# Performance work log

Measured on AMD Instinct MI355X. Metric: run time of the kernel, lower is better.

Reference implementation:

```python
import jax, jax.numpy as jnp
import numpy as np

N = 50000      # nodes
E = 800000     # edges
D_IN = 128     # input feature dim
HID = 64       # out_channels (per-head dim; concat=False -> head mean)
HEADS = 2
NEG_SLOPE = 0.2


def gat_layer(x, src, dst, Ws, Wd, a_s, a_d, b):
    # PyG GATConv, add_self_loops=False, concat=False (mean over heads)
    n = x.shape[0]
    H, C = a_s.shape
    hs = (x @ Ws).reshape(n, H, C)          # source-side features [N,H,C]
    hd = (x @ Wd).reshape(n, H, C)          # dest-side features   [N,H,C]
    als = (hs * a_s).sum(-1)                # [N,H]
    ald = (hd * a_d).sum(-1)                # [N,H]
    e = jax.nn.leaky_relu(als[src] + ald[dst], NEG_SLOPE)   # [E,H]
    # segment softmax over edges grouped by destination node
    m = jax.ops.segment_max(e, dst, num_segments=n)
    m = jax.lax.stop_gradient(jnp.where(jnp.isfinite(m), m, 0.0))
    ex = jnp.exp(e - m[dst])
    den = jax.ops.segment_sum(ex, dst, num_segments=n)
    alpha = ex / (den[dst] + 1e-16)                          # [E,H]
    out = jax.ops.segment_sum(hs[src] * alpha[:, :, None], dst, num_segments=n)
    return out.mean(axis=1) + b             # [N,C]


def setup_inputs() -> dict:
    key = jax.random.key(0)
    ks = jax.random.split(key, 32)
    d = {}
    d["x"] = jax.random.normal(ks[0], (N, D_IN), jnp.float32)
    d["edge_index"] = jax.random.randint(ks[1], (2, E), 0, N, jnp.int32)
    dins = [D_IN, HID, HID]
    i = 2
    for l in range(1, 4):
        din = dins[l - 1]
        s = 1.0 / np.sqrt(din)
        d[f"Ws{l}"] = jax.random.normal(ks[i], (din, HEADS * HID), jnp.float32) * s; i += 1
        d[f"Wd{l}"] = jax.random.normal(ks[i], (din, HEADS * HID), jnp.float32) * s; i += 1
        d[f"as{l}"] = jax.random.normal(ks[i], (HEADS, HID), jnp.float32) * 0.1; i += 1
        d[f"ad{l}"] = jax.random.normal(ks[i], (HEADS, HID), jnp.float32) * 0.1; i += 1
        d[f"b{l}"] = jnp.zeros((HID,), jnp.float32)
        d[f"Wl{l}"] = jax.random.normal(ks[i], (din, HID), jnp.float32) * s; i += 1
        d[f"bl{l}"] = jnp.zeros((HID,), jnp.float32)
    return d


def reference(x, edge_index,
              Ws1, Wd1, as1, ad1, b1, Wl1, bl1,
              Ws2, Wd2, as2, ad2, b2, Wl2, bl2,
              Ws3, Wd3, as3, ad3, b3, Wl3, bl3):
    src, dst = edge_index[0], edge_index[1]
    h = jax.nn.relu(gat_layer(x, src, dst, Ws1, Wd1, as1, ad1, b1) + x @ Wl1 + bl1)
    h = jax.nn.relu(gat_layer(h, src, dst, Ws2, Wd2, as2, ad2, b2) + h @ Wl2 + bl2)
    h = jax.nn.relu(gat_layer(h, src, dst, Ws3, Wd3, as3, ad3, b3) + h @ Wl3 + bl3)
    return h
```

## Files before the change

### kernel.cpp

```cpp
#include <hip/hip_runtime.h>
#include <hip/hip_bf16.h>

#define NN 50000
#define NE 800000
#define SCAN_BS 1024
#define SCAN_NB ((NN + SCAN_BS - 1) / SCAN_BS)
#define EB ((NE + 255) / 256)
#define GB ((NN + 63) / 64)
#define RB ((NN + 1 + 255) / 256)

typedef __attribute__((ext_vector_type(8))) __bf16 bf16x8;
typedef __attribute__((ext_vector_type(4))) float float4v;

__device__ __forceinline__ unsigned pack_bf2(float lo, float hi) {
    union { __bf16 b; unsigned short u; } a, c;
    a.b = (__bf16)lo; c.b = (__bf16)hi;
    return (unsigned)a.u | ((unsigned)c.u << 16);
}
__device__ __forceinline__ float2 unpack_bf2(unsigned v) {
    union { unsigned short u; __bf16 b; } lo, hi;
    lo.u = (unsigned short)(v & 0xffff); hi.u = (unsigned short)(v >> 16);
    return make_float2((float)lo.b, (float)hi.b);
}


__device__ __forceinline__ void convert_w_part(const float* __restrict__ Ws,
                                               const float* __restrict__ Wd,
                                               const float* __restrict__ Wl,
                                               __bf16* __restrict__ Wt, int NC, int i)
{
    if (i >= NC * 23040) return;
    int chunk = i / 23040, rem = i % 23040;
    int r = rem / 72, c = rem % 72;
    float v = 0.f;
    if (c < 64) {
        int k = chunk * 64 + c;
        if (r < 128)      v = Ws[k * 128 + r];
        else if (r < 256) v = Wd[k * 128 + (r - 128)];
        else              v = Wl[k * 64 + (r - 256)];
    }
    Wt[i] = (__bf16)v;
}

__global__ void __launch_bounds__(256)
prep_kernel(const int* __restrict__ ei, int* __restrict__ deg, int* __restrict__ rank,
            const float* __restrict__ Ws1, const float* __restrict__ Wd1,
            const float* __restrict__ Wl1, __bf16* __restrict__ Wt1,
            const float* __restrict__ Ws2, const float* __restrict__ Wd2,
            const float* __restrict__ Wl2, __bf16* __restrict__ Wt2,
            const float* __restrict__ Ws3, const float* __restrict__ Wd3,
            const float* __restrict__ Wl3, __bf16* __restrict__ Wt3)
{
    int bi = blockIdx.x;
    if (bi < EB) {
        int e = bi * 256 + threadIdx.x;
        if (e < NE) rank[e] = atomicAdd(&deg[ei[NE + e]], 1);
    } else if (bi < EB + 180) {
        convert_w_part(Ws1, Wd1, Wl1, Wt1, 2, (bi - EB) * 256 + threadIdx.x);
    } else if (bi < EB + 270) {
        convert_w_part(Ws2, Wd2, Wl2, Wt2, 1, (bi - EB - 180) * 256 + threadIdx.x);
    } else {
        convert_w_part(Ws3, Wd3, Wl3, Wt3, 1, (bi - EB - 270) * 256 + threadIdx.x);
    }
}


__global__ void __launch_bounds__(SCAN_BS)
scan12_kernel(const int* __restrict__ deg, int* __restrict__ exl,
              int* __restrict__ bsum, int* __restrict__ boff, int* __restrict__ ticket)
{
    __shared__ int sh[SCAN_BS];
    __shared__ int lastFlag;
    int t = threadIdx.x;
    int i = blockIdx.x * SCAN_BS + t;
    int v = (i < NN) ? deg[i] : 0;
    sh[t] = v;
    __syncthreads();
    for (int off = 1; off < SCAN_BS; off <<= 1) {
        int u = (t >= off) ? sh[t - off] : 0;
        __syncthreads();
        sh[t] += u;
        __syncthreads();
    }
    if (i < NN) exl[i] = sh[t] - v;
    if (t == SCAN_BS - 1) {
        bsum[blockIdx.x] = sh[t];
        __threadfence();
        lastFlag = (atomicAdd(ticket, 1) == SCAN_NB - 1);
    }
    __syncthreads();
    if (lastFlag && t < 64) {
        __threadfence();
        int l = t;
        int bv = (l < SCAN_NB) ? bsum[l] : 0;
        int own = bv;
        for (int off = 1; off < 64; off <<= 1) {
            int u = __shfl_up(bv, off);
            if (l >= off) bv += u;
        }
        if (l < SCAN_NB) boff[l] = bv - own;
    }
}


__global__ void __launch_bounds__(256)
csr_finish(const int* __restrict__ ei, const int* __restrict__ rank,
           const int* __restrict__ exl, const int* __restrict__ boff,
           int* __restrict__ row, int* __restrict__ csr_src)
{
    int bi = blockIdx.x;
    if (bi < RB) {
        int i = bi * 256 + threadIdx.x;
        if (i < NN)       row[i] = exl[i] + boff[i >> 10];
        else if (i == NN) row[i] = NE;
    } else {
        int e = (bi - RB) * 256 + threadIdx.x;
        if (e < NE) {
            int s = ei[e], d = ei[NE + e];
            csr_src[exl[d] + boff[d >> 10] + rank[e]] = s;
        }
    }
}


__device__ __forceinline__ bf16x8 load_af(const __bf16* p) { return *(const bf16x8*)p; }
__device__ __forceinline__ bf16x8 load_af(const float* p) {
    float4 u = *(const float4*)p;
    float4 v = *(const float4*)(p + 4);
    bf16x8 r;
    r[0] = (__bf16)u.x; r[1] = (__bf16)u.y; r[2] = (__bf16)u.z; r[3] = (__bf16)u.w;
    r[4] = (__bf16)v.x; r[5] = (__bf16)v.y; r[6] = (__bf16)v.z; r[7] = (__bf16)v.w;
    return r;
}

template <int K, typename TIN>
__global__ void __launch_bounds__(256, 4)
mfma_gemm(const TIN* __restrict__ xin, const __bf16* __restrict__ Wt,
          const float* __restrict__ a_s, const float* __restrict__ a_d,
          unsigned* __restrict__ hsb, float* __restrict__ lin,
          float* __restrict__ als, float* __restrict__ ald)
{
    constexpr int NPH = (K / 64) * 2;
    __shared__ __align__(16) char ldsW[160 * 144];

    const int tid  = threadIdx.x;
    const int lane = tid & 63;
    const int wave = tid >> 6;
    const int l15 = lane & 15, quad = lane >> 4;
    const int n0 = blockIdx.x * 64 + wave * 16;
    const int nA = min(n0 + l15, NN - 1);

    bf16x8 afr[K / 32];
#pragma unroll
    for (int ks = 0; ks < K / 32; ++ks)
        afr[ks] = load_af(xin + (size_t)nA * K + ks * 32 + quad * 8);

    const uint4* gW = (const uint4*)Wt;
    uint4* lw = (uint4*)ldsW;
    uint4 st[6];

#pragma unroll
    for (int i = 0; i < 6; ++i) { int idx = i * 256 + tid; if (idx < 1440) st[i] = gW[idx]; }

    float4v acc[20];
#pragma unroll
    for (int t = 0; t < 20; ++t) acc[t] = (float4v){0.f, 0.f, 0.f, 0.f};

#pragma unroll
    for (int ph = 0; ph < NPH; ++ph) {
        if (ph) __syncthreads();
#pragma unroll
        for (int i = 0; i < 6; ++i) { int idx = i * 256 + tid; if (idx < 1440) lw[idx] = st[i]; }
        __syncthreads();
        if (ph + 1 < NPH) {
            const uint4* gs = gW + (ph + 1) * 1440;
#pragma unroll
            for (int i = 0; i < 6; ++i) { int idx = i * 256 + tid; if (idx < 1440) st[i] = gs[idx]; }
        }
        const int hh = ph & 1, ch = ph >> 1;
#pragma unroll
        for (int ksh = 0; ksh < 2; ++ksh) {
#pragma unroll
            for (int tl = 0; tl < 10; ++tl) {
                bf16x8 bw = *(const bf16x8*)&ldsW[(tl * 16 + l15) * 144 + (ksh * 4 + quad) * 16];
                acc[hh * 10 + tl] =
                    __builtin_amdgcn_mfma_f32_16x16x32_bf16(bw, afr[ch * 2 + ksh], acc[hh * 10 + tl], 0, 0, 0);
            }
        }
    }

    float s0 = 0.f, s1 = 0.f, d0 = 0.f, d1 = 0.f;
#pragma unroll
    for (int t = 0; t < 4; ++t) {
        float4 as0 = *(const float4*)&a_s[t * 16 + quad * 4];
        float4 as1 = *(const float4*)&a_s[64 + t * 16 + quad * 4];
        float4 ad0 = *(const float4*)&a_d[t * 16 + quad * 4];
        float4 ad1 = *(const float4*)&a_d[64 + t * 16 + quad * 4];
        s0 += acc[t][0] * as0.x + acc[t][1] * as0.y + acc[t][2] * as0.z + acc[t][3] * as0.w;
        s1 += acc[t + 4][0] * as1.x + acc[t + 4][1] * as1.y + acc[t + 4][2] * as1.z + acc[t + 4][3] * as1.w;
        d0 += acc[t + 8][0] * ad0.x + acc[t + 8][1] * ad0.y + acc[t + 8][2] * ad0.z + acc[t + 8][3] * ad0.w;
        d1 += acc[t + 12][0] * ad1.x + acc[t + 12][1] * ad1.y + acc[t + 12][2] * ad1.z + acc[t + 12][3] * ad1.w;
    }
    s0 += __shfl_xor(s0, 16); s0 += __shfl_xor(s0, 32);
    s1 += __shfl_xor(s1, 16); s1 += __shfl_xor(s1, 32);
    d0 += __shfl_xor(d0, 16); d0 += __shfl_xor(d0, 32);
    d1 += __shfl_xor(d1, 16); d1 += __shfl_xor(d1, 32);

    int n = n0 + l15;
    if (n < NN) {
#pragma unroll
        for (int t = 0; t < 4; ++t) {
            uint4 u;
            u.x = pack_bf2(acc[t][0], acc[t + 4][0]);
            u.y = pack_bf2(acc[t][1], acc[t + 4][1]);
            u.z = pack_bf2(acc[t][2], acc[t + 4][2]);
            u.w = pack_bf2(acc[t][3], acc[t + 4][3]);
            *(uint4*)&hsb[(size_t)n * 64 + t * 16 + quad * 4] = u;
            *(float4*)&lin[(size_t)n * 64 + t * 16 + quad * 4] =
                make_float4(acc[16 + t][0], acc[16 + t][1], acc[16 + t][2], acc[16 + t][3]);
        }
        if (quad == 0) *(float2*)&als[(size_t)n * 2] = make_float2(s0, s1);
        if (quad == 1) *(float2*)&ald[(size_t)n * 2] = make_float2(d0, d1);
    }
}


__device__ __forceinline__ float2 edge_w(const float* __restrict__ als, int s,
                                         float ad0, float ad1)
{
    float2 al = *(const float2*)&als[s * 2];
    float e0 = al.x + ad0; e0 = (e0 >= 0.f) ? e0 : 0.2f * e0;
    float e1 = al.y + ad1; e1 = (e1 >= 0.f) ? e1 : 0.2f * e1;
    return make_float2(__expf(e0), __expf(e1));
}

__device__ __forceinline__ void store_q(float* p, float v0, float v1, float v2, float v3) {
    *(float4*)p = make_float4(v0, v1, v2, v3);
}
__device__ __forceinline__ void store_q(__bf16* p, float v0, float v1, float v2, float v3) {
    *(uint2*)p = make_uint2(pack_bf2(v0, v1), pack_bf2(v2, v3));
}

template <typename TO>
__global__ void __launch_bounds__(256, 8)
gat_aggregate(const int* __restrict__ row, const int* __restrict__ csr_src,
              const float* __restrict__ als, const float* __restrict__ ald,
              const unsigned* __restrict__ hsb, const float* __restrict__ lin,
              const float* __restrict__ b, const float* __restrict__ bl,
              TO* __restrict__ out)
{
    int w = (blockIdx.x * 256 + threadIdx.x) >> 6;
    int lane = threadIdx.x & 63;
    int q = lane >> 4;
    int l15 = lane & 15;
    if (w >= NN) return;
    int p0 = row[w], p1 = row[w + 1];
    float ad0 = ald[w * 2 + 0];
    float ad1 = ald[w * 2 + 1];

    float a0[4] = {0.f, 0.f, 0.f, 0.f};
    float a1[4] = {0.f, 0.f, 0.f, 0.f};
    float den0 = 0.f, den1 = 0.f;

    for (int p = p0 + q; p < p1; p += 16) {
#pragma unroll
        for (int j = 0; j < 4; ++j) {
            int pp = p + 4 * j;
            bool live = (pp < p1);
            int s = csr_src[live ? pp : p0];
            float2 e = edge_w(als, s, ad0, ad1);
            if (!live) e = make_float2(0.f, 0.f);
            uint4 g = *(const uint4*)&hsb[(size_t)s * 64 + 4 * l15];
            den0 += e.x; den1 += e.y;
            float2 h;
            h = unpack_bf2(g.x); a0[0] += e.x * h.x; a1[0] += e.y * h.y;
            h = unpack_bf2(g.y); a0[1] += e.x * h.x; a1[1] += e.y * h.y;
            h = unpack_bf2(g.z); a0[2] += e.x * h.x; a1[2] += e.y * h.y;
            h = unpack_bf2(g.w); a0[3] += e.x * h.x; a1[3] += e.y * h.y;
        }
    }

#pragma unroll
    for (int i = 0; i < 4; ++i) {
        a0[i] += __shfl_xor(a0[i], 16); a0[i] += __shfl_xor(a0[i], 32);
        a1[i] += __shfl_xor(a1[i], 16); a1[i] += __shfl_xor(a1[i], 32);
    }
    den0 += __shfl_xor(den0, 16); den0 += __shfl_xor(den0, 32);
    den1 += __shfl_xor(den1, 16); den1 += __shfl_xor(den1, 32);

    if (q == 0) {
        int c0 = 4 * l15;
        float r0 = 1.f / (den0 + 1e-16f);
        float r1 = 1.f / (den1 + 1e-16f);
        float4 lv = *(const float4*)&lin[(size_t)w * 64 + c0];
        float v0 = 0.5f * (a0[0] * r0 + a1[0] * r1) + b[c0 + 0] + bl[c0 + 0] + lv.x;
        float v1 = 0.5f * (a0[1] * r0 + a1[1] * r1) + b[c0 + 1] + bl[c0 + 1] + lv.y;
        float v2 = 0.5f * (a0[2] * r0 + a1[2] * r1) + b[c0 + 2] + bl[c0 + 2] + lv.z;
        float v3 = 0.5f * (a0[3] * r0 + a1[3] * r1) + b[c0 + 3] + bl[c0 + 3] + lv.w;
        store_q(&out[(size_t)w * 64 + c0],
                fmaxf(v0, 0.f), fmaxf(v1, 0.f), fmaxf(v2, 0.f), fmaxf(v3, 0.f));
    }
}


extern "C" void kernel_launch(void* const* d_in, const int* in_sizes, int n_in,
                              void* d_out, int out_size, void* d_ws, size_t ws_size,
                              hipStream_t stream)
{
    const float* x  = (const float*)d_in[0];
    const int*   ei = (const int*)d_in[1];
    const float* Ws[3]; const float* Wd[3]; const float* As[3]; const float* Ad[3];
    const float* Bb[3]; const float* Wl[3]; const float* Bl[3];
    for (int l = 0; l < 3; ++l) {
        int base = 2 + 7 * l;
        Ws[l] = (const float*)d_in[base + 0];
        Wd[l] = (const float*)d_in[base + 1];
        As[l] = (const float*)d_in[base + 2];
        Ad[l] = (const float*)d_in[base + 3];
        Bb[l] = (const float*)d_in[base + 4];
        Wl[l] = (const float*)d_in[base + 5];
        Bl[l] = (const float*)d_in[base + 6];
    }

    float* ws = (float*)d_ws;
    unsigned* hsb = (unsigned*)ws;
    float* lin  = (float*)(hsb + (size_t)NN * 64);
    float* als  = lin + (size_t)NN * 64;
    float* ald  = als + (size_t)NN * 2;
    __bf16* hb  = (__bf16*)(ald + (size_t)NN * 2);
    __bf16* Wt1 = hb + (size_t)NN * 64;
    __bf16* Wt2 = Wt1 + 2 * 320 * 72;
    __bf16* Wt3 = Wt2 + 320 * 72;
    int* row     = (int*)(Wt3 + 320 * 72);
    int* deg     = row + (NN + 1);
    int* ticket  = deg + NN;
    int* rank    = ticket + 1;
    int* exl     = rank + NE;
    int* bsum    = exl + NN;
    int* boff    = bsum + SCAN_NB;
    int* csr_src = boff + SCAN_NB;

    const int WB = (NN * 64 + 255) / 256;

    hipMemsetAsync(deg, 0, sizeof(int) * (NN + 1), stream);
    prep_kernel<<<EB + 360, 256, 0, stream>>>(ei, deg, rank,
        Ws[0], Wd[0], Wl[0], Wt1,
        Ws[1], Wd[1], Wl[1], Wt2,
        Ws[2], Wd[2], Wl[2], Wt3);
    scan12_kernel<<<SCAN_NB, SCAN_BS, 0, stream>>>(deg, exl, bsum, boff, ticket);
    csr_finish<<<RB + EB, 256, 0, stream>>>(ei, rank, exl, boff, row, csr_src);

    for (int l = 0; l < 3; ++l) {
        if (l == 0) {
            mfma_gemm<128, float><<<GB, 256, 0, stream>>>(
                x, Wt1, As[0], Ad[0], hsb, lin, als, ald);
        } else {
            const __bf16* wt = (l == 1) ? Wt2 : Wt3;
            mfma_gemm<64, __bf16><<<GB, 256, 0, stream>>>(
                hb, wt, As[l], Ad[l], hsb, lin, als, ald);
        }
        if (l == 2) {
            gat_aggregate<float><<<WB, 256, 0, stream>>>(
                row, csr_src, als, ald, hsb, lin, Bb[l], Bl[l], (float*)d_out);
        } else {
            gat_aggregate<__bf16><<<WB, 256, 0, stream>>>(
                row, csr_src, als, ald, hsb, lin, Bb[l], Bl[l], hb);
        }
    }
}
```

Baseline: 365.5 us.

## Fuse all stages into one persistent cooperative mega-kernel with grid syncs

Replaces the memset plus separate prep, scan, CSR-finish, GEMM and aggregation launches with a single cooperative kernel that walks each stage with grid-stride loops separated by grid.sync. Layer-1 GEMM is co-scheduled with the CSR row/scatter phase, and the block-offset scan becomes a serial single-thread pass. This removes launch gaps and tail idling between kernels, at the cost of grid-wide barrier overhead and occupancy being capped by the GEMM's register/LDS needs for the aggregation phases as well.

Measured after the change: 1.040 ms. 185% more time.

```diff
diff --git a/kernel.cpp b/kernel.cpp
--- a/kernel.cpp
+++ b/kernel.cpp
@@ -1,13 +1,18 @@
 #include <hip/hip_runtime.h>
 #include <hip/hip_bf16.h>
+#include <hip/hip_cooperative_groups.h>
+
+namespace cg = cooperative_groups;
 
 #define NN 50000
 #define NE 800000
-#define SCAN_BS 1024
-#define SCAN_NB ((NN + SCAN_BS - 1) / SCAN_BS)
-#define EB ((NE + 255) / 256)
-#define GB ((NN + 63) / 64)
-#define RB ((NN + 1 + 255) / 256)
+#define NCH 196
+#define CVU 360
+#define ZU  196
+#define EBU 3125
+#define GBU 782
+#define RBU 196
+#define AGU 12500
 
 typedef __attribute__((ext_vector_type(8))) __bf16 bf16x8;
 typedef __attribute__((ext_vector_type(4))) float float4v;
@@ -23,13 +28,21 @@
     return make_float2((float)lo.b, (float)hi.b);
 }
 
+struct MegaArgs {
+    const float* x; const int* ei;
+    const float* Ws[3]; const float* Wd[3]; const float* Wl[3];
+    const float* as[3]; const float* ad[3]; const float* bb[3]; const float* bl[3];
+    __bf16* Wt1; __bf16* Wt2; __bf16* Wt3;
+    unsigned* hsb; float* lin; float* als; float* ald; __bf16* hb;
+    int* row; int* deg; int* rank; int* exl; int* bsum; int* boff; int* csr_src;
+    float* out;
+};
 
 __device__ __forceinline__ void convert_w_part(const float* __restrict__ Ws,
                                                const float* __restrict__ Wd,
                                                const float* __restrict__ Wl,
-                                               __bf16* __restrict__ Wt, int NC, int i)
-{
-    if (i >= NC * 23040) return;
+                                               __bf16* __restrict__ Wt, int i)
+{
     int chunk = i / 23040, rem = i % 23040;
     int r = rem / 72, c = rem % 72;
     float v = 0.f;
@@ -42,87 +55,6 @@
     Wt[i] = (__bf16)v;
 }
 
-__global__ void __launch_bounds__(256)
-prep_kernel(const int* __restrict__ ei, int* __restrict__ deg, int* __restrict__ rank,
-            const float* __restrict__ Ws1, const float* __restrict__ Wd1,
-            const float* __restrict__ Wl1, __bf16* __restrict__ Wt1,
-            const float* __restrict__ Ws2, const float* __restrict__ Wd2,
-            const float* __restrict__ Wl2, __bf16* __restrict__ Wt2,
-            const float* __restrict__ Ws3, const float* __restrict__ Wd3,
-            const float* __restrict__ Wl3, __bf16* __restrict__ Wt3)
-{
-    int bi = blockIdx.x;
-    if (bi < EB) {
-        int e = bi * 256 + threadIdx.x;
-        if (e < NE) rank[e] = atomicAdd(&deg[ei[NE + e]], 1);
-    } else if (bi < EB + 180) {
-        convert_w_part(Ws1, Wd1, Wl1, Wt1, 2, (bi - EB) * 256 + threadIdx.x);
-    } else if (bi < EB + 270) {
-        convert_w_part(Ws2, Wd2, Wl2, Wt2, 1, (bi - EB - 180) * 256 + threadIdx.x);
-    } else {
-        convert_w_part(Ws3, Wd3, Wl3, Wt3, 1, (bi - EB - 270) * 256 + threadIdx.x);
-    }
-}
-
-
-__global__ void __launch_bounds__(SCAN_BS)
-scan12_kernel(const int* __restrict__ deg, int* __restrict__ exl,
-              int* __restrict__ bsum, int* __restrict__ boff, int* __restrict__ ticket)
-{
-    __shared__ int sh[SCAN_BS];
-    __shared__ int lastFlag;
-    int t = threadIdx.x;
-    int i = blockIdx.x * SCAN_BS + t;
-    int v = (i < NN) ? deg[i] : 0;
-    sh[t] = v;
-    __syncthreads();
-    for (int off = 1; off < SCAN_BS; off <<= 1) {
-        int u = (t >= off) ? sh[t - off] : 0;
-        __syncthreads();
-        sh[t] += u;
-        __syncthreads();
-    }
-    if (i < NN) exl[i] = sh[t] - v;
-    if (t == SCAN_BS - 1) {
-        bsum[blockIdx.x] = sh[t];
-        __threadfence();
-        lastFlag = (atomicAdd(ticket, 1) == SCAN_NB - 1);
-    }
-    __syncthreads();
-    if (lastFlag && t < 64) {
-        __threadfence();
-        int l = t;
-        int bv = (l < SCAN_NB) ? bsum[l] : 0;
-        int own = bv;
-        for (int off = 1; off < 64; off <<= 1) {
-            int u = __shfl_up(bv, off);
-            if (l >= off) bv += u;
-        }
-        if (l < SCAN_NB) boff[l] = bv - own;
-    }
-}
-
-
-__global__ void __launch_bounds__(256)
-csr_finish(const int* __restrict__ ei, const int* __restrict__ rank,
-           const int* __restrict__ exl, const int* __restrict__ boff,
-           int* __restrict__ row, int* __restrict__ csr_src)
-{
-    int bi = blockIdx.x;
-    if (bi < RB) {
-        int i = bi * 256 + threadIdx.x;
-        if (i < NN)       row[i] = exl[i] + boff[i >> 10];
-        else if (i == NN) row[i] = NE;
-    } else {
-        int e = (bi - RB) * 256 + threadIdx.x;
-        if (e < NE) {
-            int s = ei[e], d = ei[NE + e];
-            csr_src[exl[d] + boff[d >> 10] + rank[e]] = s;
-        }
-    }
-}
-
-
 __device__ __forceinline__ bf16x8 load_af(const __bf16* p) { return *(const bf16x8*)p; }
 __device__ __forceinline__ bf16x8 load_af(const float* p) {
     float4 u = *(const float4*)p;
@@ -134,20 +66,18 @@
 }
 
 template <int K, typename TIN>
-__global__ void __launch_bounds__(256, 4)
-mfma_gemm(const TIN* __restrict__ xin, const __bf16* __restrict__ Wt,
-          const float* __restrict__ a_s, const float* __restrict__ a_d,
-          unsigned* __restrict__ hsb, float* __restrict__ lin,
-          float* __restrict__ als, float* __restrict__ ald)
+__device__ __forceinline__ void gemm_tile(int item, const TIN* __restrict__ xin,
+        const __bf16* __restrict__ Wt,
+        const float* __restrict__ a_s, const float* __restrict__ a_d,
+        unsigned* __restrict__ hsb, float* __restrict__ lin,
+        float* __restrict__ als, float* __restrict__ ald, char* ldsW)
 {
     constexpr int NPH = (K / 64) * 2;
-    __shared__ __align__(16) char ldsW[160 * 144];
-
     const int tid  = threadIdx.x;
     const int lane = tid & 63;
     const int wave = tid >> 6;
     const int l15 = lane & 15, quad = lane >> 4;
-    const int n0 = blockIdx.x * 64 + wave * 16;
+    const int n0 = item * 64 + wave * 16;
     const int nA = min(n0 + l15, NN - 1);
 
     bf16x8 afr[K / 32];
@@ -168,7 +98,7 @@
 
 #pragma unroll
     for (int ph = 0; ph < NPH; ++ph) {
-        if (ph) __syncthreads();
+        __syncthreads();
 #pragma unroll
         for (int i = 0; i < 6; ++i) { int idx = i * 256 + tid; if (idx < 1440) lw[idx] = st[i]; }
         __syncthreads();
@@ -188,6 +118,7 @@
             }
         }
     }
+    __syncthreads();
 
     float s0 = 0.f, s1 = 0.f, d0 = 0.f, d1 = 0.f;
 #pragma unroll
@@ -224,7 +155,6 @@
     }
 }
 
-
 __device__ __forceinline__ float2 edge_w(const float* __restrict__ als, int s,
                                          float ad0, float ad1)
 {
@@ -233,7 +163,6 @@
     float e1 = al.y + ad1; e1 = (e1 >= 0.f) ? e1 : 0.2f * e1;
     return make_float2(__expf(e0), __expf(e1));
 }
-
 __device__ __forceinline__ void store_q(float* p, float v0, float v1, float v2, float v3) {
     *(float4*)p = make_float4(v0, v1, v2, v3);
 }
@@ -242,18 +171,16 @@
 }
 
 template <typename TO>
-__global__ void __launch_bounds__(256, 8)
-gat_aggregate(const int* __restrict__ row, const int* __restrict__ csr_src,
-              const float* __restrict__ als, const float* __restrict__ ald,
-              const unsigned* __restrict__ hsb, const float* __restrict__ lin,
-              const float* __restrict__ b, const float* __restrict__ bl,
-              TO* __restrict__ out)
-{
-    int w = (blockIdx.x * 256 + threadIdx.x) >> 6;
+__device__ __forceinline__ void agg_node(int w,
+        const int* __restrict__ row, const int* __restrict__ csr_src,
+        const float* __restrict__ als, const float* __restrict__ ald,
+        const unsigned* __restrict__ hsb, const float* __restrict__ lin,
+        const float* __restrict__ b, const float* __restrict__ bl,
+        TO* __restrict__ out)
+{
     int lane = threadIdx.x & 63;
     int q = lane >> 4;
     int l15 = lane & 15;
-    if (w >= NN) return;
     int p0 = row[w], p1 = row[w + 1];
     float ad0 = ald[w * 2 + 0];
     float ad1 = ald[w * 2 + 1];
@@ -302,69 +229,158 @@
     }
 }
 
+__global__ void __launch_bounds__(256, 4)
+mega_kernel(MegaArgs A)
+{
+    __shared__ __align__(16) char lds[160 * 144];
+    cg::grid_group grid = cg::this_grid();
+    const int G = gridDim.x;
+    const int tid = threadIdx.x;
+
+    for (int u = blockIdx.x; u < CVU + ZU; u += G) {
+        if (u < CVU) {
+            int i = u * 256 + tid;
+            if (i < 46080)      convert_w_part(A.Ws[0], A.Wd[0], A.Wl[0], A.Wt1, i);
+            else if (i < 69120) convert_w_part(A.Ws[1], A.Wd[1], A.Wl[1], A.Wt2, i - 46080);
+            else                convert_w_part(A.Ws[2], A.Wd[2], A.Wl[2], A.Wt3, i - 69120);
+        } else {
+            int i = (u - CVU) * 256 + tid;
+            if (i < NN) A.deg[i] = 0;
+        }
+    }
+    grid.sync();
+
+    for (int u = blockIdx.x; u < EBU; u += G) {
+        int e = u * 256 + tid;
+        if (e < NE) A.rank[e] = atomicAdd(&A.deg[A.ei[NE + e]], 1);
+    }
+    grid.sync();
+
+    {
+        int* sh = (int*)lds;
+        for (int u = blockIdx.x; u < NCH; u += G) {
+            int i = u * 256 + tid;
+            int v = (i < NN) ? A.deg[i] : 0;
+            sh[tid] = v;
+            __syncthreads();
+            for (int off = 1; off < 256; off <<= 1) {
+                int t = (tid >= off) ? sh[tid - off] : 0;
+                __syncthreads();
+                sh[tid] += t;
+                __syncthreads();
+            }
+            if (i < NN) A.exl[i] = sh[tid] - v;
+            if (tid == 255) A.bsum[u] = sh[255];
+            __syncthreads();
+        }
+    }
+    grid.sync();
+
+    if (blockIdx.x == 0 && tid == 0) {
+        int run = 0;
+        for (int c = 0; c < NCH; ++c) { A.boff[c] = run; run += A.bsum[c]; }
+    }
+    grid.sync();
+
+    for (int u = blockIdx.x; u < GBU + RBU + EBU; u += G) {
+        if (u < GBU) {
+            gemm_tile<128, float>(u, A.x, A.Wt1, A.as[0], A.ad[0],
+                                  A.hsb, A.lin, A.als, A.ald, lds);
+        } else if (u < GBU + RBU) {
+            int i = (u - GBU) * 256 + tid;
+            if (i < NN)       A.row[i] = A.exl[i] + A.boff[i >> 8];
+            else if (i == NN) A.row[i] = NE;
+        } else {
+            int e = (u - GBU - RBU) * 256 + tid;
+            if (e < NE) {
+                int s = A.ei[e], d = A.ei[NE + e];
+                A.csr_src[A.exl[d] + A.boff[d >> 8] + A.rank[e]] = s;
+            }
+        }
+    }
+    grid.sync();
+
+    for (int u = blockIdx.x; u < AGU; u += G) {
+        int w = u * 4 + (tid >> 6);
+        if (w < NN) agg_node<__bf16>(w, A.row, A.csr_src, A.als, A.ald,
+                                     A.hsb, A.lin, A.bb[0], A.bl[0], A.hb);
+    }
+    grid.sync();
+
+    for (int u = blockIdx.x; u < GBU; u += G)
+        gemm_tile<64, __bf16>(u, A.hb, A.Wt2, A.as[1], A.ad[1],
+                              A.hsb, A.lin, A.als, A.ald, lds);
+    grid.sync();
+
+    for (int u = blockIdx.x; u < AGU; u += G) {
+        int w = u * 4 + (tid >> 6);
+        if (w < NN) agg_node<__bf16>(w, A.row, A.csr_src, A.als, A.ald,
+                                     A.hsb, A.lin, A.bb[1], A.bl[1], A.hb);
+    }
+    grid.sync();
+
+    for (int u = blockIdx.x; u < GBU; u += G)
+        gemm_tile<64, __bf16>(u, A.hb, A.Wt3, A.as[2], A.ad[2],
+                              A.hsb, A.lin, A.als, A.ald, lds);
+    grid.sync();
+
+    for (int u = blockIdx.x; u < AGU; u += G) {
+        int w = u * 4 + (tid >> 6);
+        if (w < NN) agg_node<float>(w, A.row, A.csr_src, A.als, A.ald,
+                                    A.hsb, A.lin, A.bb[2], A.bl[2], A.out);
+    }
+}
+
 
 extern "C" void kernel_launch(void* const* d_in, const int* in_sizes, int n_in,
                               void* d_out, int out_size, void* d_ws, size_t ws_size,
                               hipStream_t stream)
 {
-    const float* x  = (const float*)d_in[0];
-    const int*   ei = (const int*)d_in[1];
-    const float* Ws[3]; const float* Wd[3]; const float* As[3]; const float* Ad[3];
-    const float* Bb[3]; const float* Wl[3]; const float* Bl[3];
+    MegaArgs A;
+    A.x  = (const float*)d_in[0];
+    A.ei = (const int*)d_in[1];
     for (int l = 0; l < 3; ++l) {
         int base = 2 + 7 * l;
-        Ws[l] = (const float*)d_in[base + 0];
-        Wd[l] = (const float*)d_in[base + 1];
-        As[l] = (const float*)d_in[base + 2];
-        Ad[l] = (const float*)d_in[base + 3];
-        Bb[l] = (const float*)d_in[base + 4];
-        Wl[l] = (const float*)d_in[base + 5];
-        Bl[l] = (const float*)d_in[base + 6];
+        A.Ws[l] = (const float*)d_in[base + 0];
+        A.Wd[l] = (const float*)d_in[base + 1];
+        A.as[l] = (const float*)d_in[base + 2];
+        A.ad[l] = (const float*)d_in[base + 3];
+        A.bb[l] = (const float*)d_in[base + 4];
+        A.Wl[l] = (const float*)d_in[base + 5];
+        A.bl[l] = (const float*)d_in[base + 6];
     }
 
     float* ws = (float*)d_ws;
-    unsigned* hsb = (unsigned*)ws;
-    float* lin  = (float*)(hsb + (size_t)NN * 64);
-    float* als  = lin + (size_t)NN * 64;
-    float* ald  = als + (size_t)NN * 2;
-    __bf16* hb  = (__bf16*)(ald + (size_t)NN * 2);
-    __bf16* Wt1 = hb + (size_t)NN * 64;
-    __bf16* Wt2 = Wt1 + 2 * 320 * 72;
-    __bf16* Wt3 = Wt2 + 320 * 72;
-    int* row     = (int*)(Wt3 + 320 * 72);
-    int* deg     = row + (NN + 1);
-    int* ticket  = deg + NN;
-    int* rank    = ticket + 1;
-    int* exl     = rank + NE;
-    int* bsum    = exl + NN;
-    int* boff    = bsum + SCAN_NB;
-    int* csr_src = boff + SCAN_NB;
-
-    const int WB = (NN * 64 + 255) / 256;
-
-    hipMemsetAsync(deg, 0, sizeof(int) * (NN + 1), stream);
-    prep_kernel<<<EB + 360, 256, 0, stream>>>(ei, deg, rank,
-        Ws[0], Wd[0], Wl[0], Wt1,
-        Ws[1], Wd[1], Wl[1], Wt2,
-        Ws[2], Wd[2], Wl[2], Wt3);
-    scan12_kernel<<<SCAN_NB, SCAN_BS, 0, stream>>>(deg, exl, bsum, boff, ticket);
-    csr_finish<<<RB + EB, 256, 0, stream>>>(ei, rank, exl, boff, row, csr_src);
-
-    for (int l = 0; l < 3; ++l) {
-        if (l == 0) {
-            mfma_gemm<128, float><<<GB, 256, 0, stream>>>(
-                x, Wt1, As[0], Ad[0], hsb, lin, als, ald);
-        } else {
-            const __bf16* wt = (l == 1) ? Wt2 : Wt3;
-            mfma_gemm<64, __bf16><<<GB, 256, 0, stream>>>(
-                hb, wt, As[l], Ad[l], hsb, lin, als, ald);
-        }
-        if (l == 2) {
-            gat_aggregate<float><<<WB, 256, 0, stream>>>(
-                row, csr_src, als, ald, hsb, lin, Bb[l], Bl[l], (float*)d_out);
-        } else {
-            gat_aggregate<__bf16><<<WB, 256, 0, stream>>>(
-                row, csr_src, als, ald, hsb, lin, Bb[l], Bl[l], hb);
-        }
-    }
-}
+    A.hsb = (unsigned*)ws;
+    A.lin = (float*)(A.hsb + (size_t)NN * 64);
+    A.als = A.lin + (size_t)NN * 64;
+    A.ald = A.als + (size_t)NN * 2;
+    A.hb  = (__bf16*)(A.ald + (size_t)NN * 2);
+    A.Wt1 = A.hb + (size_t)NN * 64;
+    A.Wt2 = A.Wt1 + 2 * 320 * 72;
+    A.Wt3 = A.Wt2 + 320 * 72;
+    A.row = (int*)(A.Wt3 + 320 * 72);
+    A.deg = A.row + (NN + 1);
+    A.rank = A.deg + NN;
+    A.exl  = A.rank + NE;
+    A.bsum = A.exl + NN;
+    A.boff = A.bsum + NCH;
+    A.csr_src = A.boff + NCH;
+    A.out = (float*)d_out;
+
+    static int grid = 0;
+    if (grid == 0) {
+        int bpc = 0, ncu = 0, dev = 0;
+        hipGetDevice(&dev);
+        hipOccupancyMaxActiveBlocksPerMultiprocessor(&bpc, (const void*)mega_kernel, 256, 0);
+        hipDeviceGetAttribute(&ncu, hipDeviceAttributeMultiprocessorCount, dev);
+        if (bpc < 1) bpc = 1;
+        if (ncu < 1) ncu = 256;
+        grid = bpc * ncu;
+        if (grid > 4096) grid = 4096;
+    }
+
+    void* kargs[] = { (void*)&A };
+    hipLaunchCooperativeKernel((const void*)mega_kernel, dim3(grid), dim3(256),
+                               kargs, 0, stream);
+}
```
